# Kernel tuning notes

Measured on AMD Instinct MI355X. Metric: run time of the kernel, lower is better.

The kernel has to match this reference:

```python
import math
import jax, jax.numpy as jnp
from jax import lax
import numpy as np

STRIDES = (8, 16, 32)            # p3, p4, p5
ANCHOR_STRIDE_SCALE = 8
ASPECT_RATIOS = (0.5, 1.0, 2.0)  # A = 3
NMS_THRESH = 0.6
PRE_NMS_TOPK = 400
POST_NMS_TOPK = 50
BBOX_CLAMP = 4.135166556742356   # log(1000/16)


def setup_inputs() -> dict:
    key = jax.random.key(0)
    ks = jax.random.split(key, 8)
    C = 256
    inp = {
        "p3": jax.random.normal(ks[0], (8, C, 128, 128), jnp.float32),
        "p4": jax.random.normal(ks[1], (8, C, 64, 64), jnp.float32),
        "p5": jax.random.normal(ks[2], (8, C, 32, 32), jnp.float32),
        # fan-in scaled weights so logits/deltas stay in a sane range
        "w_stem": jax.random.normal(ks[3], (C, C, 3, 3), jnp.float32) * (1.0 / math.sqrt(C * 9)),
        "b_stem": jnp.zeros((C,), jnp.float32),
        "w_obj": jax.random.normal(ks[4], (3, C, 1, 1), jnp.float32) * (1.0 / math.sqrt(C)),
        "b_obj": jnp.zeros((3,), jnp.float32),
        "w_box": jax.random.normal(ks[5], (12, C, 1, 1), jnp.float32) * (0.01 / math.sqrt(C)),
        "b_box": jnp.zeros((12,), jnp.float32),
    }
    return inp


def _conv(x, w, b, pad):
    y = lax.conv_general_dilated(x, w, (1, 1), pad,
                                 dimension_numbers=("NCHW", "OIHW", "NCHW"))
    return y + b[None, :, None, None]


def _make_anchors(H, W, stride):
    # anchor centers at (x+0.5)*stride ; base size = stride * anchor_stride_scale
    xs = (jnp.arange(W, dtype=jnp.float32) + 0.5) * stride
    ys = (jnp.arange(H, dtype=jnp.float32) + 0.5) * stride
    cx, cy = jnp.meshgrid(xs, ys)              # (H, W), row-major matches H*W flatten
    cx = cx.reshape(-1)
    cy = cy.reshape(-1)
    size = float(stride * ANCHOR_STRIDE_SCALE)
    per_ratio = []
    for r in ASPECT_RATIOS:
        w = size / math.sqrt(r)
        h = size * math.sqrt(r)
        per_ratio.append(jnp.stack([cx - w / 2, cy - h / 2, cx + w / 2, cy + h / 2], axis=-1))
    return jnp.stack(per_ratio, axis=1).reshape(-1, 4)  # (H*W*A, 4)


def _decode(deltas, anchors):
    aw = anchors[:, 2] - anchors[:, 0]
    ah = anchors[:, 3] - anchors[:, 1]
    acx = anchors[:, 0] + 0.5 * aw
    acy = anchors[:, 1] + 0.5 * ah
    dx, dy = deltas[:, 0], deltas[:, 1]
    dw = jnp.clip(deltas[:, 2], -BBOX_CLAMP, BBOX_CLAMP)
    dh = jnp.clip(deltas[:, 3], -BBOX_CLAMP, BBOX_CLAMP)
    pcx = acx + dx * aw
    pcy = acy + dy * ah
    pw = aw * jnp.exp(dw)
    ph = ah * jnp.exp(dh)
    return jnp.stack([pcx - 0.5 * pw, pcy - 0.5 * ph,
                      pcx + 0.5 * pw, pcy + 0.5 * ph], axis=-1)


def _nms_keep(boxes, thresh):
    # boxes already sorted by descending score; greedy class-agnostic NMS
    N = boxes.shape[0]
    x1, y1, x2, y2 = boxes[:, 0], boxes[:, 1], boxes[:, 2], boxes[:, 3]
    area = jnp.maximum(x2 - x1, 0.0) * jnp.maximum(y2 - y1, 0.0)
    ix1 = jnp.maximum(x1[:, None], x1[None, :])
    iy1 = jnp.maximum(y1[:, None], y1[None, :])
    ix2 = jnp.minimum(x2[:, None], x2[None, :])
    iy2 = jnp.minimum(y2[:, None], y2[None, :])
    inter = jnp.maximum(ix2 - ix1, 0.0) * jnp.maximum(iy2 - iy1, 0.0)
    iou = inter / jnp.maximum(area[:, None] + area[None, :] - inter, 1e-8)  # (N, N)
    idx = jnp.arange(N)

    def body(keep, i):
        suppress = (iou[i] > thresh) & keep[i] & (idx > i)
        return keep & ~suppress, 0

    keep, _ = lax.scan(body, jnp.ones((N,), bool), idx)
    return keep


def _proposals_one_image(logits, deltas, anchors):
    # logits: (N,), deltas: (N, 4), anchors: (N, 4)
    k = min(PRE_NMS_TOPK, logits.shape[0])
    scores, top_idx = lax.top_k(logits, k)
    boxes = _decode(deltas[top_idx], anchors[top_idx])
    keep = _nms_keep(boxes, NMS_THRESH)
    masked = jnp.where(keep, scores, -jnp.inf)
    _, kidx = lax.top_k(masked, POST_NMS_TOPK)
    return boxes[kidx]  # (POST_NMS_TOPK, 4)


def _rpn_level(feat, w_stem, b_stem, w_obj, b_obj, w_box, b_box, stride):
    B, _, H, W = feat.shape
    x = jax.nn.relu(_conv(feat, w_stem, b_stem, "SAME"))       # stem: 3x3 conv + ReLU
    obj = _conv(x, w_obj, b_obj, "VALID")                      # (B, A, H, W)
    box = _conv(x, w_box, b_box, "VALID")                      # (B, 4A, H, W)
    A = obj.shape[1]
    obj = obj.transpose(0, 2, 3, 1).reshape(B, H * W * A)       # (B, HWA)
    box = box.transpose(0, 2, 3, 1).reshape(B, H * W * A, 4)    # (B, HWA, 4)
    anchors = _make_anchors(H, W, stride)                       # (HWA, 4)
    return jax.vmap(lambda o, d: _proposals_one_image(o, d, anchors))(obj, box)


def reference(p3, p4, p5, w_stem, b_stem, w_obj, b_obj, w_box, b_box):
    out = []
    for feat, stride in zip((p3, p4, p5), STRIDES):
        out.append(_rpn_level(feat, w_stem, b_stem, w_obj, b_obj, w_box, b_box, stride))
    # (B, 3 * POST_NMS_TOPK, 4) absolute XYXY proposals, concatenated across levels
    return jnp.concatenate(out, axis=1)
```

## Files before the change

### kernel.cpp

```cpp
#include <hip/hip_runtime.h>
#include <math.h>
#include <stdint.h>

#define BBOX_CLAMP 4.135166556742356f
#define SQH 0.70710678118654752f
#define SQ2 1.41421356237309515f

typedef __attribute__((ext_vector_type(8))) short s8b;
typedef __attribute__((ext_vector_type(4))) float f32x4;
typedef __attribute__((ext_vector_type(4))) short s4b;

__device__ __forceinline__ unsigned okey(float f){
  unsigned u = __float_as_uint(f);
  return (u & 0x80000000u) ? ~u : (u | 0x80000000u);
}
__device__ __forceinline__ unsigned short f2bf(float f){
  unsigned u = __float_as_uint(f);
  unsigned r = (u + 0x7FFFu + ((u >> 16) & 1u)) >> 16;
  return (unsigned short)r;
}
__device__ __forceinline__ float bf2f(unsigned short h){
  return __uint_as_float(((unsigned)h) << 16);
}

__global__ void k_wsplit(const float* __restrict__ w,
                         unsigned short* __restrict__ whi, unsigned short* __restrict__ wlo){
  const int ck = blockIdx.x;
  const int cout = threadIdx.x;
  const int cin = ck / 9, tap = ck - cin*9;
  const float x = w[cout*2304 + ck];
  const unsigned short h = f2bf(x);
  const unsigned short lo2 = f2bf(x - bf2f(h));
  const int slice = cin >> 5, g = (cin >> 3) & 3, j = cin & 7;
  const size_t off = ((((size_t)tap*8 + slice)*4 + g)*256 + cout)*8 + j;
  whi[off] = h; wlo[off] = lo2;
}

__global__ __launch_bounds__(256, 2) void k_stem_mfma(
    const float* __restrict__ p3f, const float* __restrict__ p4f, const float* __restrict__ p5f,
    const unsigned short* __restrict__ whi, const unsigned short* __restrict__ wlo,
    const float* __restrict__ bstem,
    const float* __restrict__ wobj, const float* __restrict__ bobj,
    const float* __restrict__ wbox, const float* __restrict__ bbox,
    float* __restrict__ sc3, float* __restrict__ dl3,
    float* __restrict__ sc4, float* __restrict__ dl4,
    float* __restrict__ sc5, float* __restrict__ dl5)
{
  __shared__ __align__(16) unsigned char smem[32640];
  unsigned short* Abuf = reinterpret_cast<unsigned short*>(smem);
  float* part = reinterpret_cast<float*>(smem);

  const int tid = threadIdx.x;
  const int l = tid & 63, w = tid >> 6;
  const int li = l & 15, g = l >> 4;
  const int p = w >> 1, c = w & 1;

  int id = blockIdx.x;
  const float* feat; float* scores; float* deltas; int H, W, bx, by, b;
  if (id < 1024){ feat=p3f; scores=sc3; deltas=dl3; H=128; W=128;
      bx = id & 3; by = (id >> 2) & 31; b = id >> 7; }
  else if (id < 1280){ id -= 1024; feat=p4f; scores=sc4; deltas=dl4; H=64; W=64;
      bx = id & 1; by = (id >> 1) & 15; b = id >> 5; }
  else { id -= 1280; feat=p5f; scores=sc5; deltas=dl5; H=32; W=32;
      bx = 0; by = id & 7; b = id >> 3; }
  const int px0 = bx*32, py0 = by*4;
  const size_t HW = (size_t)H*W;
  const float* fb = feat + (size_t)b*256*HW;

  const int gr = tid / 34, gc = tid - gr*34;
  const int row = py0 + gr - 1, col = px0 + gc - 1;
  const bool inb = (tid < 204) && row >= 0 && row < H && col >= 0 && col < W;
  const bool lact = (tid < 204);
  const float* gA = fb + ((size_t)(inb ? row : 0)*W + (inb ? col : 0));

  f32x4 acc[4][8];
#pragma unroll
  for (int m=0;m<4;++m)
#pragma unroll
    for (int cg=0;cg<8;++cg) acc[m][cg] = (f32x4){0.f,0.f,0.f,0.f};

  for (int slice = 0; slice < 8; ++slice){
    __syncthreads();
    const float* gs = gA + (size_t)slice*32*HW;
#pragma unroll
    for (int ch = 0; ch < 8; ++ch){
      float x0=0.f, x1=0.f, x2=0.f, x3=0.f;
      if (inb){
        x0 = gs[(size_t)(ch*4+0)*HW];
        x1 = gs[(size_t)(ch*4+1)*HW];
        x2 = gs[(size_t)(ch*4+2)*HW];
        x3 = gs[(size_t)(ch*4+3)*HW];
      }
      if (lact){
        const unsigned short h0=f2bf(x0), h1=f2bf(x1), h2=f2bf(x2), h3=f2bf(x3);
        s4b hv; hv[0]=(short)h0; hv[1]=(short)h1; hv[2]=(short)h2; hv[3]=(short)h3;
        s4b lv; lv[0]=(short)f2bf(x0-bf2f(h0)); lv[1]=(short)f2bf(x1-bf2f(h1));
                lv[2]=(short)f2bf(x2-bf2f(h2)); lv[3]=(short)f2bf(x3-bf2f(h3));
        *reinterpret_cast<s4b*>(&Abuf[tid*40 + ch*4]) = hv;
        *reinterpret_cast<s4b*>(&Abuf[8160 + tid*40 + ch*4]) = lv;
      }
    }
    __syncthreads();

    for (int tap = 0; tap < 9; ++tap){
      const int dr = tap/3 - 1, dc = tap - (tap/3)*3 - 1;
      s8b ah[4], al[4];
#pragma unroll
      for (int m = 0; m < 4; ++m){
        const int rm = 2*p + (m >> 1), cm = m & 1;
        const int aoff = ((rm+dr+1)*34 + cm*16 + li + dc + 1)*40 + g*8;
        ah[m] = *reinterpret_cast<const s8b*>(&Abuf[aoff]);
        al[m] = *reinterpret_cast<const s8b*>(&Abuf[8160 + aoff]);
      }
#pragma unroll
      for (int chunk = 0; chunk < 2; ++chunk){
        s8b bh[4], bl[4];
#pragma unroll
        for (int cg4 = 0; cg4 < 4; ++cg4){
          const int cout = c*128 + (chunk*4 + cg4)*16 + li;
          const int woff = ((((tap*8 + slice)*4 + g)*256) + cout)*8;
          bh[cg4] = *reinterpret_cast<const s8b*>(&whi[woff]);
          bl[cg4] = *reinterpret_cast<const s8b*>(&wlo[woff]);
        }
#pragma unroll
        for (int m = 0; m < 4; ++m){
#pragma unroll
          for (int cg4 = 0; cg4 < 4; ++cg4)
            acc[m][chunk*4+cg4] = __builtin_amdgcn_mfma_f32_16x16x32_bf16(ah[m], bh[cg4], acc[m][chunk*4+cg4], 0, 0, 0);
#pragma unroll
          for (int cg4 = 0; cg4 < 4; ++cg4)
            acc[m][chunk*4+cg4] = __builtin_amdgcn_mfma_f32_16x16x32_bf16(ah[m], bl[cg4], acc[m][chunk*4+cg4], 0, 0, 0);
#pragma unroll
          for (int cg4 = 0; cg4 < 4; ++cg4)
            acc[m][chunk*4+cg4] = __builtin_amdgcn_mfma_f32_16x16x32_bf16(al[m], bh[cg4], acc[m][chunk*4+cg4], 0, 0, 0);
        }
      }
    }
  }

#pragma unroll
  for (int cg = 0; cg < 8; ++cg){
    const float bsv = bstem[c*128 + cg*16 + li];
#pragma unroll
    for (int m = 0; m < 4; ++m)
#pragma unroll
      for (int r = 0; r < 4; ++r)
        acc[m][cg][r] = fmaxf(acc[m][cg][r] + bsv, 0.f);
  }

  __syncthreads();

#pragma unroll
  for (int oc = 0; oc < 15; ++oc){
    float wv[8];
#pragma unroll
    for (int cg = 0; cg < 8; ++cg){
      const int cc = c*128 + cg*16 + li;
      wv[cg] = (oc < 3) ? wobj[oc*256 + cc] : wbox[(oc-3)*256 + cc];
    }
#pragma unroll
    for (int m = 0; m < 4; ++m){
#pragma unroll
      for (int r = 0; r < 4; ++r){
        float t = acc[m][0][r] * wv[0];
#pragma unroll
        for (int cg = 1; cg < 8; ++cg) t = fmaf(acc[m][cg][r], wv[cg], t);
        t += __shfl_xor(t, 1, 64);
        t += __shfl_xor(t, 2, 64);
        t += __shfl_xor(t, 4, 64);
        t += __shfl_xor(t, 8, 64);
        if (li == 0)
          part[(w*64 + m*16 + g*4 + r)*17 + oc] = t;
      }
    }
  }
  __syncthreads();

  {
    const int p_idx = tid & 127, half = tid >> 7;
    const int mg = p_idx >> 4, i16 = p_idx & 15;
    const int rm = mg >> 1, cm = mg & 1;
    const int pp = mg >> 2, ml = mg & 3;
    const int hh = py0 + rm, ww = px0 + cm*16 + i16;
    const size_t loc = (size_t)hh*W + ww;
    const int oce = half ? 15 : 8;
    for (int oc = half*8; oc < oce; ++oc){
      float s = part[((2*pp)*64 + ml*16 + i16)*17 + oc]
              + part[((2*pp+1)*64 + ml*16 + i16)*17 + oc];
      s += (oc < 3) ? bobj[oc] : bbox[oc-3];
      if (oc < 3) scores[(size_t)b*HW*3 + loc*3 + oc] = s;
      else        deltas[(size_t)b*HW*12 + loc*12 + (oc-3)] = s;
    }
  }
}

__global__ __launch_bounds__(1024) void k_select(
    const float* __restrict__ sc3, const float* __restrict__ sc4, const float* __restrict__ sc5,
    const float* __restrict__ dl3, const float* __restrict__ dl4, const float* __restrict__ dl5,
    float* __restrict__ out)
{
  const int lvl = blockIdx.x >> 3;
  const int b   = blockIdx.x & 7;
  int N, W; float stride; const float* sc; const float* dl;
  if (lvl==0){ N=49152; W=128; stride=8.f;  sc=sc3; dl=dl3; }
  else if (lvl==1){ N=12288; W=64; stride=16.f; sc=sc4; dl=dl4; }
  else { N=3072; W=32; stride=32.f; sc=sc5; dl=dl5; }
  sc += (size_t)b*N;
  dl += (size_t)b*(size_t)(N/3)*12;

  __shared__ unsigned hist[256];
  __shared__ unsigned s_prefix;
  __shared__ int s_need;
  __shared__ int s_cntc;
  __shared__ unsigned long long cand[1024];
  __shared__ unsigned long long srt[400];
  __shared__ float bx1[400], by1[400], bx2[400], by2[400], bar_[400];
  __shared__ unsigned long long mask[400][7];
  __shared__ int olist[50];

  const int t = threadIdx.x;

  if (t==0){ s_prefix=0u; s_need=400; }
  for (int pass=0; pass<4; ++pass){
    const int shift = 24 - 8*pass;
    if (t<256) hist[t]=0u;
    __syncthreads();
    const unsigned pref = s_prefix;
    for (int i=t; i<N; i+=1024){
      const unsigned k = okey(sc[i]);
      if (pass==0 || (k >> (shift+8)) == pref)
        atomicAdd(&hist[(k>>shift)&255u], 1u);
    }
    __syncthreads();
    if (t==0){
      int need = s_need, cum=0, bsel=0;
      for (int bb=255; bb>=0; --bb){
        const int h = (int)hist[bb];
        if (cum + h >= need){ bsel=bb; break; }
        cum += h;
      }
      s_prefix = (pref<<8) | (unsigned)bsel;
      s_need = need - cum;
    }
    __syncthreads();
  }
  const unsigned K = s_prefix;

  if (t==0) s_cntc = 0;
  cand[t] = 0ull;
  __syncthreads();
  for (int i=t; i<N; i+=1024){
    const unsigned k = okey(sc[i]);
    if (k >= K){
      const int pos = atomicAdd(&s_cntc, 1);
      if (pos < 1024)
        cand[pos] = ((unsigned long long)k<<32) | (unsigned long long)(0xFFFFFFFFu - (unsigned)i);
    }
  }
  __syncthreads();

  {
    const int cnt = (s_cntc < 1024) ? s_cntc : 1024;
    if (t < cnt){
      const unsigned long long mine = cand[t];
      int r = 0;
      for (int j = 0; j < cnt; ++j) r += (cand[j] > mine) ? 1 : 0;
      if (r < 400) srt[r] = mine;
    }
  }
  __syncthreads();

  if (t < 400){
    const unsigned long long cc = srt[t];
    const int gi = (int)(0xFFFFFFFFu - (unsigned)(cc & 0xFFFFFFFFull));
    const int loc = gi/3, a = gi - loc*3;
    const int hh = loc / W, ww = loc - hh*W;
    const float cx = (ww + 0.5f)*stride, cy = (hh + 0.5f)*stride;
    const float size = stride*8.f;
    const float sq = (a==0) ? SQH : ((a==1) ? 1.f : SQ2);
    const float hw_ = 0.5f*(size/sq);
    const float hv_ = 0.5f*(size*sq);
    const float ax1 = cx - hw_, ax2 = cx + hw_;
    const float ay1 = cy - hv_, ay2 = cy + hv_;
    const float aw = ax2 - ax1, ah = ay2 - ay1;
    const float acx = ax1 + 0.5f*aw, acy = ay1 + 0.5f*ah;
    const float* dd = dl + (size_t)loc*12 + a*4;
    const float dx = dd[0], dy = dd[1];
    const float dw = fminf(fmaxf(dd[2], -BBOX_CLAMP), BBOX_CLAMP);
    const float dh = fminf(fmaxf(dd[3], -BBOX_CLAMP), BBOX_CLAMP);
    const float pcx = acx + dx*aw;
    const float pcy = acy + dy*ah;
    const float pw = aw*expf(dw);
    const float ph = ah*expf(dh);
    const float x1 = pcx - 0.5f*pw, y1 = pcy - 0.5f*ph;
    const float x2 = pcx + 0.5f*pw, y2 = pcy + 0.5f*ph;
    bx1[t]=x1; by1[t]=y1; bx2[t]=x2; by2[t]=y2;
    bar_[t] = fmaxf(x2-x1, 0.f)*fmaxf(y2-y1, 0.f);
  }
  __syncthreads();

  for (int task=t; task<2800; task+=1024){
    const int i = task/7, w = task - (task/7)*7;
    unsigned long long m = 0ull;
    const float xi1=bx1[i], yi1=by1[i], xi2=bx2[i], yi2=by2[i], ai=bar_[i];
    const int j0 = w<<6;
    const int js = (j0 > i+1) ? j0 : (i+1);
    const int je = (j0+64 < 400) ? (j0+64) : 400;
    for (int j=js; j<je; ++j){
      const float ix1 = fmaxf(xi1, bx1[j]);
      const float iy1 = fmaxf(yi1, by1[j]);
      const float ix2 = fminf(xi2, bx2[j]);
      const float iy2 = fminf(yi2, by2[j]);
      const float inter = fmaxf(ix2-ix1, 0.f)*fmaxf(iy2-iy1, 0.f);
      const float iou = inter / fmaxf(ai + bar_[j] - inter, 1e-8f);
      if (iou > 0.6f) m |= (1ull << (j - j0));
    }
    mask[i][w] = m;
  }
  __syncthreads();

  if (t==0){
    unsigned long long keepw[7];
#pragma unroll
    for (int w=0;w<7;++w) keepw[w] = ~0ull;
    for (int i=0;i<400;++i){
      if ((keepw[i>>6] >> (i&63)) & 1ull){
#pragma unroll
        for (int w=0;w<7;++w) keepw[w] &= ~mask[i][w];
      }
    }
    int cnt=0;
    for (int i=0;i<400 && cnt<50;++i) if ( (keepw[i>>6]>>(i&63)) & 1ull) olist[cnt++]=i;
    for (int i=0;i<400 && cnt<50;++i) if (!((keepw[i>>6]>>(i&63)) & 1ull)) olist[cnt++]=i;
  }
  __syncthreads();

  if (t < 50){
    const int j = olist[t];
    float* o = out + (size_t)b*600 + (size_t)(lvl*50 + t)*4;
    o[0]=bx1[j]; o[1]=by1[j]; o[2]=bx2[j]; o[3]=by2[j];
  }
}

extern "C" void kernel_launch(void* const* d_in, const int* in_sizes, int n_in,
                              void* d_out, int out_size, void* d_ws, size_t ws_size,
                              hipStream_t stream) {
  (void)in_sizes; (void)n_in; (void)out_size; (void)ws_size;
  const float* p3     = (const float*)d_in[0];
  const float* p4     = (const float*)d_in[1];
  const float* p5     = (const float*)d_in[2];
  const float* w_stem = (const float*)d_in[3];
  const float* b_stem = (const float*)d_in[4];
  const float* w_obj  = (const float*)d_in[5];
  const float* b_obj  = (const float*)d_in[6];
  const float* w_box  = (const float*)d_in[7];
  const float* b_box  = (const float*)d_in[8];
  float* out = (float*)d_out;

  unsigned short* whi = (unsigned short*)d_ws;
  unsigned short* wlo = whi + 589824;
  float* sc3 = (float*)(wlo + 589824);
  float* sc4 = sc3 + 393216;
  float* sc5 = sc4 + 98304;
  float* dl3 = sc5 + 24576;
  float* dl4 = dl3 + 1572864;
  float* dl5 = dl4 + 393216;

  k_wsplit<<<dim3(2304), dim3(256), 0, stream>>>(w_stem, whi, wlo);

  k_stem_mfma<<<dim3(1344), dim3(256), 0, stream>>>(
      p3, p4, p5, whi, wlo, b_stem, w_obj, b_obj, w_box, b_box,
      sc3, dl3, sc4, dl4, sc5, dl5);

  k_select<<<dim3(24), dim3(1024), 0, stream>>>(sc3, sc4, sc5, dl3, dl4, dl5, out);
}
```

Before: 787.2 us.

## Switch stem conv to 32x32x16 bf16 MFMA tiles with priority hints

Rewrites the stem 3x3 conv inner loop to use 32x32x16 bf16 MFMA instructions instead of 16x16x32, tiling each wave as 2 pixel rows by 4 groups of 32 output channels. The larger tiles need fewer A/B operand loads from LDS and global memory per FLOP. The loop also wraps the MFMA sequences in s_setprio, and the 1x1 head reduction and partial-sum layout are remapped to match the new accumulator layout. This risks different register pressure, a wider shuffle reduction, and mistakes in the output index mapping.

```diff
diff --git a/kernel.cpp b/kernel.cpp
--- a/kernel.cpp
+++ b/kernel.cpp
@@ -8,6 +8,7 @@
 
 typedef __attribute__((ext_vector_type(8))) short s8b;
 typedef __attribute__((ext_vector_type(4))) float f32x4;
+typedef __attribute__((ext_vector_type(16))) float f32x16;
 typedef __attribute__((ext_vector_type(4))) short s4b;
 
 __device__ __forceinline__ unsigned okey(float f){
@@ -52,7 +53,7 @@
 
   const int tid = threadIdx.x;
   const int l = tid & 63, w = tid >> 6;
-  const int li = l & 15, g = l >> 4;
+  const int li32 = l & 31, hi = l >> 5;
   const int p = w >> 1, c = w & 1;
 
   int id = blockIdx.x;
@@ -73,11 +74,13 @@
   const bool lact = (tid < 204);
   const float* gA = fb + ((size_t)(inb ? row : 0)*W + (inb ? col : 0));
 
-  f32x4 acc[4][8];
-#pragma unroll
-  for (int m=0;m<4;++m)
-#pragma unroll
-    for (int cg=0;cg<8;++cg) acc[m][cg] = (f32x4){0.f,0.f,0.f,0.f};
+  f32x16 acc[2][4];
+#pragma unroll
+  for (int m=0;m<2;++m)
+#pragma unroll
+    for (int n=0;n<4;++n)
+#pragma unroll
+      for (int r=0;r<16;++r) acc[m][n][r] = 0.f;
 
   for (int slice = 0; slice < 8; ++slice){
     __syncthreads();
@@ -104,73 +107,73 @@
 
     for (int tap = 0; tap < 9; ++tap){
       const int dr = tap/3 - 1, dc = tap - (tap/3)*3 - 1;
-      s8b ah[4], al[4];
-#pragma unroll
-      for (int m = 0; m < 4; ++m){
-        const int rm = 2*p + (m >> 1), cm = m & 1;
-        const int aoff = ((rm+dr+1)*34 + cm*16 + li + dc + 1)*40 + g*8;
-        ah[m] = *reinterpret_cast<const s8b*>(&Abuf[aoff]);
-        al[m] = *reinterpret_cast<const s8b*>(&Abuf[8160 + aoff]);
-      }
-#pragma unroll
-      for (int chunk = 0; chunk < 2; ++chunk){
-        s8b bh[4], bl[4];
-#pragma unroll
-        for (int cg4 = 0; cg4 < 4; ++cg4){
-          const int cout = c*128 + (chunk*4 + cg4)*16 + li;
-          const int woff = ((((tap*8 + slice)*4 + g)*256) + cout)*8;
-          bh[cg4] = *reinterpret_cast<const s8b*>(&whi[woff]);
-          bl[cg4] = *reinterpret_cast<const s8b*>(&wlo[woff]);
+#pragma unroll
+      for (int khalf = 0; khalf < 2; ++khalf){
+        s8b ah[2], al[2];
+#pragma unroll
+        for (int m = 0; m < 2; ++m){
+          const int aoff = ((2*p + m + dr + 1)*34 + li32 + dc + 1)*40 + khalf*16 + hi*8;
+          ah[m] = *reinterpret_cast<const s8b*>(&Abuf[aoff]);
+          al[m] = *reinterpret_cast<const s8b*>(&Abuf[8160 + aoff]);
         }
-#pragma unroll
-        for (int m = 0; m < 4; ++m){
-#pragma unroll
-          for (int cg4 = 0; cg4 < 4; ++cg4)
-            acc[m][chunk*4+cg4] = __builtin_amdgcn_mfma_f32_16x16x32_bf16(ah[m], bh[cg4], acc[m][chunk*4+cg4], 0, 0, 0);
-#pragma unroll
-          for (int cg4 = 0; cg4 < 4; ++cg4)
-            acc[m][chunk*4+cg4] = __builtin_amdgcn_mfma_f32_16x16x32_bf16(ah[m], bl[cg4], acc[m][chunk*4+cg4], 0, 0, 0);
-#pragma unroll
-          for (int cg4 = 0; cg4 < 4; ++cg4)
-            acc[m][chunk*4+cg4] = __builtin_amdgcn_mfma_f32_16x16x32_bf16(al[m], bh[cg4], acc[m][chunk*4+cg4], 0, 0, 0);
+        const int grp = khalf*2 + hi;
+#pragma unroll
+        for (int n = 0; n < 4; ++n){
+          const int cout = c*128 + n*32 + li32;
+          const int woff = ((((tap*8 + slice)*4 + grp)*256) + cout)*8;
+          const s8b bh = *reinterpret_cast<const s8b*>(&whi[woff]);
+          const s8b bl = *reinterpret_cast<const s8b*>(&wlo[woff]);
+          __builtin_amdgcn_s_setprio(1);
+#pragma unroll
+          for (int m = 0; m < 2; ++m){
+            acc[m][n] = __builtin_amdgcn_mfma_f32_32x32x16_bf16(ah[m], bh, acc[m][n], 0, 0, 0);
+            acc[m][n] = __builtin_amdgcn_mfma_f32_32x32x16_bf16(ah[m], bl, acc[m][n], 0, 0, 0);
+            acc[m][n] = __builtin_amdgcn_mfma_f32_32x32x16_bf16(al[m], bh, acc[m][n], 0, 0, 0);
+          }
+          __builtin_amdgcn_s_setprio(0);
         }
       }
     }
   }
 
 #pragma unroll
-  for (int cg = 0; cg < 8; ++cg){
-    const float bsv = bstem[c*128 + cg*16 + li];
-#pragma unroll
-    for (int m = 0; m < 4; ++m)
-#pragma unroll
-      for (int r = 0; r < 4; ++r)
-        acc[m][cg][r] = fmaxf(acc[m][cg][r] + bsv, 0.f);
+  for (int n = 0; n < 4; ++n){
+    const float bsv = bstem[c*128 + n*32 + li32];
+#pragma unroll
+    for (int m = 0; m < 2; ++m)
+#pragma unroll
+      for (int r = 0; r < 16; ++r)
+        acc[m][n][r] = fmaxf(acc[m][n][r] + bsv, 0.f);
   }
 
   __syncthreads();
 
 #pragma unroll
   for (int oc = 0; oc < 15; ++oc){
-    float wv[8];
-#pragma unroll
-    for (int cg = 0; cg < 8; ++cg){
-      const int cc = c*128 + cg*16 + li;
-      wv[cg] = (oc < 3) ? wobj[oc*256 + cc] : wbox[(oc-3)*256 + cc];
-    }
-#pragma unroll
-    for (int m = 0; m < 4; ++m){
-#pragma unroll
-      for (int r = 0; r < 4; ++r){
+    float wv[4];
+#pragma unroll
+    for (int n = 0; n < 4; ++n){
+      const int cc = c*128 + n*32 + li32;
+      wv[n] = (oc < 3) ? wobj[oc*256 + cc] : wbox[(oc-3)*256 + cc];
+    }
+#pragma unroll
+    for (int m = 0; m < 2; ++m){
+#pragma unroll
+      for (int r = 0; r < 16; ++r){
         float t = acc[m][0][r] * wv[0];
-#pragma unroll
-        for (int cg = 1; cg < 8; ++cg) t = fmaf(acc[m][cg][r], wv[cg], t);
+        t = fmaf(acc[m][1][r], wv[1], t);
+        t = fmaf(acc[m][2][r], wv[2], t);
+        t = fmaf(acc[m][3][r], wv[3], t);
         t += __shfl_xor(t, 1, 64);
         t += __shfl_xor(t, 2, 64);
         t += __shfl_xor(t, 4, 64);
         t += __shfl_xor(t, 8, 64);
-        if (li == 0)
-          part[(w*64 + m*16 + g*4 + r)*17 + oc] = t;
+        t += __shfl_xor(t, 16, 64);
+        if (li32 == 0){
+          const int pxcol = (r & 3) + 8*(r >> 2) + 4*hi;
+          const int px = (2*p + m)*32 + pxcol;
+          part[(c*128 + px)*17 + oc] = t;
+        }
       }
     }
   }
@@ -178,15 +181,12 @@
 
   {
     const int p_idx = tid & 127, half = tid >> 7;
-    const int mg = p_idx >> 4, i16 = p_idx & 15;
-    const int rm = mg >> 1, cm = mg & 1;
-    const int pp = mg >> 2, ml = mg & 3;
-    const int hh = py0 + rm, ww = px0 + cm*16 + i16;
+    const int hh = py0 + (p_idx >> 5), ww = px0 + (p_idx & 31);
     const size_t loc = (size_t)hh*W + ww;
     const int oce = half ? 15 : 8;
     for (int oc = half*8; oc < oce; ++oc){
-      float s = part[((2*pp)*64 + ml*16 + i16)*17 + oc]
-              + part[((2*pp+1)*64 + ml*16 + i16)*17 + oc];
+      float s = part[(0*128 + p_idx)*17 + oc]
+              + part[(1*128 + p_idx)*17 + oc];
       s += (oc < 3) ? bobj[oc] : bbox[oc-3];
       if (oc < 3) scores[(size_t)b*HW*3 + loc*3 + oc] = s;
       else        deltas[(size_t)b*HW*12 + loc*12 + (oc-3)] = s;
```

Result: slower. 1.340 ms (+70.2%).
